# Performance work log

Measured on AMD Instinct MI355X. Metric: run time of the kernel, lower is better.

## Reference

```python
import jax, jax.numpy as jnp
import numpy as np

B, T, D = 2, 2048, 1024
H, DK, DV, NH = 8, 128, 256, 2  # heads, key dim, value dim (expand_v=2), num_householder
CONV = 4
INTER = 2816
EPS = 1e-6


def rmsnorm(x, w):
    return x * jax.lax.rsqrt(jnp.mean(x * x, -1, keepdims=True) + EPS) * w


def l2norm(x):
    return x * jax.lax.rsqrt(jnp.sum(x * x, -1, keepdims=True) + 1e-6)


def causal_conv_silu(x, w):
    # depthwise causal conv1d with silu activation; x: [B,T,C], w: [C,K]
    K = w.shape[1]
    xp = jnp.pad(x, ((0, 0), (K - 1, 0), (0, 0)))
    y = sum(xp[:, i:i + x.shape[1], :] * w[:, i] for i in range(K))
    return jax.nn.silu(y)


def setup_inputs():
    key = jax.random.key(0)
    ks = jax.random.split(key, 16)
    s = 0.02
    return {
        "hidden_states": jax.random.normal(ks[0], (B, T, D), jnp.float32),
        "attn_norm_w": jnp.ones((D,), jnp.float32),
        "Wq": jax.random.normal(ks[1], (D, H * DK), jnp.float32) * s,
        "Wk": jax.random.normal(ks[2], (D, NH * H * DK), jnp.float32) * s,
        "Wv": jax.random.normal(ks[3], (D, NH * H * DV), jnp.float32) * s,
        "Wb": jax.random.normal(ks[4], (D, H * NH), jnp.float32) * s,
        "Wa": jax.random.normal(ks[5], (D, H), jnp.float32) * s,
        "A_log": jnp.log(jax.random.uniform(ks[6], (H,), jnp.float32, 1.0, 16.0)),
        "dt_bias": jax.random.normal(ks[7], (H,), jnp.float32) * 0.5,
        "conv_q_w": jax.random.normal(ks[8], (H * DK, CONV), jnp.float32) * 0.5,
        "conv_k_w": jax.random.normal(ks[9], (NH * H * DK, CONV), jnp.float32) * 0.5,
        "conv_v_w": jax.random.normal(ks[10], (NH * H * DV, CONV), jnp.float32) * 0.5,
        "Wg": jax.random.normal(ks[11], (D, H * DV), jnp.float32) * s,
        "o_norm_w": jnp.ones((DV,), jnp.float32),
        "Wo": jax.random.normal(ks[12], (H * DV, D), jnp.float32) * s,
        "mlp_norm_w": jnp.ones((D,), jnp.float32),
        "Wgate": jax.random.normal(ks[13], (D, 2 * INTER), jnp.float32) * s,
        "Wdown": jax.random.normal(ks[14], (INTER, D), jnp.float32) * s,
    }


def reference(hidden_states, attn_norm_w, Wq, Wk, Wv, Wb, Wa, A_log, dt_bias,
              conv_q_w, conv_k_w, conv_v_w, Wg, o_norm_w, Wo,
              mlp_norm_w, Wgate, Wdown):
    residual = hidden_states
    x = rmsnorm(hidden_states, attn_norm_w)

    # projections + short conv + silu, then L2-normalized q/k (gated delta rule)
    q = l2norm(causal_conv_silu(x @ Wq, conv_q_w).reshape(B, T, H, DK))
    k = l2norm(causal_conv_silu(x @ Wk, conv_k_w).reshape(B, T, NH, H, DK))
    v = causal_conv_silu(x @ Wv, conv_v_w).reshape(B, T, NH, H, DV)
    beta = jax.nn.sigmoid(x @ Wb).reshape(B, T, H, NH)
    g = -jnp.exp(A_log) * jax.nn.softplus(x @ Wa + dt_bias)  # [B,T,H] log-decay

    def step(S, inp):
        q_t, k_t, v_t, b_t, g_t = inp
        # forget gate applied once per token, then NH Householder delta-rule updates
        S = S * jnp.exp(g_t)[..., None, None]  # S: [B,H,DK,DV]
        for j in range(NH):
            kj, vj, bj = k_t[:, j], v_t[:, j], b_t[..., j]
            kS = jnp.einsum('bhk,bhkv->bhv', kj, S)
            S = S + bj[..., None, None] * jnp.einsum('bhk,bhv->bhkv', kj, vj - kS)
        o_t = jnp.einsum('bhk,bhkv->bhv', q_t, S)
        return S, o_t

    S0 = jnp.zeros((B, H, DK, DV), x.dtype)
    xs = (jnp.swapaxes(q, 0, 1), jnp.swapaxes(k, 0, 1), jnp.swapaxes(v, 0, 1),
          jnp.swapaxes(beta, 0, 1), jnp.swapaxes(g, 0, 1))
    _, o = jax.lax.scan(step, S0, xs)  # [T,B,H,DV]
    o = jnp.swapaxes(o, 0, 1)

    # gated RMSNorm output gate + output projection
    gate = (x @ Wg).reshape(B, T, H, DV)
    o = rmsnorm(o, o_norm_w) * jax.nn.silu(gate)
    hidden = residual + o.reshape(B, T, H * DV) @ Wo

    # GatedMLP (swiglu)
    y = rmsnorm(hidden, mlp_norm_w)
    gate_m, up = jnp.split(y @ Wgate, 2, -1)
    return hidden + (jax.nn.silu(gate_m) * up) @ Wdown
```

## Files before the change

kernel.cpp:

```cpp
#include <hip/hip_runtime.h>
#include <hip/hip_bf16.h>
#include <math.h>

#define Bq 2
#define Tq 2048
#define Dq 1024
#define Hq 8
#define DKq 128
#define DVq 256
#define NHq 2
#define BTq (Bq*Tq)
#define INTERq 2816

typedef __hip_bfloat16 bf16;
typedef short bfv8 __attribute__((ext_vector_type(8)));
typedef float f32v4 __attribute__((ext_vector_type(4)));

__device__ __forceinline__ float b2f(bf16 v){ return __bfloat162float(v); }
__device__ __forceinline__ bf16 f2b(float v){ return __float2bfloat16(v); }

__device__ __forceinline__ int is_f32(const unsigned* magic){ return magic[0] == 0x3F800000u; }

__device__ __forceinline__ float ldin(const void* p, int f32, size_t i){
  return f32 ? ((const float*)p)[i] : b2f(((const bf16*)p)[i]);
}

__device__ __forceinline__ float block_reduce_sum(float v, float* red){
  #pragma unroll
  for (int off = 32; off > 0; off >>= 1) v += __shfl_down(v, off, 64);
  int lane = threadIdx.x & 63, wid = threadIdx.x >> 6;
  if (lane == 0) red[wid] = v;
  __syncthreads();
  int nw = (blockDim.x + 63) >> 6;
  float tot = 0.f;
  for (int i = 0; i < nw; i++) tot += red[i];
  return tot;
}

__global__ __launch_bounds__(256) void rmsnorm_kernel(const void* __restrict__ in, int in_mode,
    const void* __restrict__ w, const unsigned* __restrict__ magic,
    bf16* __restrict__ out){
  __shared__ float red[4];
  int f32 = is_f32(magic);
  int inf32 = in_mode ? 1 : f32;
  size_t row = blockIdx.x;
  float xv[4];
  float ss = 0.f;
  #pragma unroll
  for (int j = 0; j < 4; j++){
    int i = threadIdx.x + j*256;
    float v = ldin(in, inf32, row*Dq + i);
    xv[j] = v; ss += v*v;
  }
  float tot = block_reduce_sum(ss, red);
  float sc = rsqrtf(tot / (float)Dq + 1e-6f);
  #pragma unroll
  for (int j = 0; j < 4; j++){
    int i = threadIdx.x + j*256;
    out[row*Dq + i] = f2b(xv[j] * sc * ldin(w, f32, i));
  }
}

__global__ __launch_bounds__(256) void wsplit_kernel(
    const void* __restrict__ W, const unsigned* __restrict__ magic,
    bf16* __restrict__ hi, bf16* __restrict__ lo, int K, int N){
  __shared__ float tile[32][33];
  int f32 = is_f32(magic);
  int n0 = blockIdx.x * 32, k0 = blockIdx.y * 32;
  int tx = threadIdx.x & 31, ty = threadIdx.x >> 5;
  #pragma unroll
  for (int r = 0; r < 4; r++){
    int kr = ty + r*8;
    tile[kr][tx] = ldin(W, f32, (size_t)(k0 + kr)*N + n0 + tx);
  }
  __syncthreads();
  #pragma unroll
  for (int r = 0; r < 4; r++){
    int nr = ty + r*8;
    float v = tile[tx][nr];
    bf16 h = f2b(v);
    size_t idx = (size_t)(n0 + nr)*K + k0 + tx;
    hi[idx] = h;
    if (f32) lo[idx] = f2b(v - b2f(h));
  }
}

__global__ __launch_bounds__(256) void gemm_mfma_kernel(
    const bf16* __restrict__ A, const bf16* __restrict__ WThi, const bf16* __restrict__ WTlo,
    const unsigned* __restrict__ magic,
    const void* __restrict__ res, int res_mode,
    void* __restrict__ out, int out_mode,
    int M, int N, int K){
  int f32 = is_f32(magic);
  int tid = threadIdx.x;
  int lane = tid & 63, w = tid >> 6;
  int wm = w >> 1, wn = w & 1;
  int l15 = lane & 15, quad = lane >> 4;
  size_t bm = (size_t)blockIdx.x * 128, bn = (size_t)blockIdx.y * 128;

  f32v4 acc[4][4];
  #pragma unroll
  for (int mt = 0; mt < 4; mt++)
    #pragma unroll
    for (int nt = 0; nt < 4; nt++) acc[mt][nt] = 0.f;

  const bf16* Ab = A    + (bm + wm*64 + l15)*(size_t)K + quad*8;
  const bf16* Bh = WThi + (bn + wn*64 + l15)*(size_t)K + quad*8;
  const bf16* Bl = WTlo + (bn + wn*64 + l15)*(size_t)K + quad*8;

  if (f32){
    for (int k0 = 0; k0 < K; k0 += 32){
      bfv8 a[4];
      #pragma unroll
      for (int mt = 0; mt < 4; mt++)
        a[mt] = *(const bfv8*)(Ab + (size_t)mt*16*K + k0);
      #pragma unroll
      for (int nt = 0; nt < 4; nt++){
        bfv8 bh = *(const bfv8*)(Bh + (size_t)nt*16*K + k0);
        bfv8 bl = *(const bfv8*)(Bl + (size_t)nt*16*K + k0);
        #pragma unroll
        for (int mt = 0; mt < 4; mt++){
          acc[mt][nt] = __builtin_amdgcn_mfma_f32_16x16x32_bf16(a[mt], bh, acc[mt][nt], 0, 0, 0);
          acc[mt][nt] = __builtin_amdgcn_mfma_f32_16x16x32_bf16(a[mt], bl, acc[mt][nt], 0, 0, 0);
        }
      }
    }
  } else {
    for (int k0 = 0; k0 < K; k0 += 32){
      bfv8 a[4];
      #pragma unroll
      for (int mt = 0; mt < 4; mt++)
        a[mt] = *(const bfv8*)(Ab + (size_t)mt*16*K + k0);
      #pragma unroll
      for (int nt = 0; nt < 4; nt++){
        bfv8 bh = *(const bfv8*)(Bh + (size_t)nt*16*K + k0);
        #pragma unroll
        for (int mt = 0; mt < 4; mt++)
          acc[mt][nt] = __builtin_amdgcn_mfma_f32_16x16x32_bf16(a[mt], bh, acc[mt][nt], 0, 0, 0);
      }
    }
  }
  #pragma unroll
  for (int mt = 0; mt < 4; mt++)
    #pragma unroll
    for (int nt = 0; nt < 4; nt++)
      #pragma unroll
      for (int r = 0; r < 4; r++){
        size_t row = bm + wm*64 + mt*16 + quad*4 + r;
        size_t col = bn + wn*64 + nt*16 + l15;
        float v = acc[mt][nt][r];
        if (res_mode == 1) v += ldin(res, f32, row*N + col);
        else if (res_mode == 2) v += ((const float*)res)[row*N + col];
        if (out_mode == 0) ((float*)out)[row*N + col] = v;
        else if (out_mode == 1) ((bf16*)out)[row*N + col] = f2b(v);
        else { if (f32) ((float*)out)[row*N + col] = v; else ((bf16*)out)[row*N + col] = f2b(v); }
      }
}

__global__ __launch_bounds__(256) void betag_kernel(
    const bf16* __restrict__ x, const void* __restrict__ Wb, const void* __restrict__ Wa,
    const void* __restrict__ A_log, const void* __restrict__ dt_bias,
    const unsigned* __restrict__ magic,
    float* __restrict__ beta, float* __restrict__ eg){
  __shared__ float xs[Dq];
  int f32 = is_f32(magic);
  size_t bt = blockIdx.x;
  for (int i = threadIdx.x; i < Dq; i += 256) xs[i] = b2f(x[bt*Dq + i]);
  __syncthreads();
  int wv = threadIdx.x >> 6, lane = threadIdx.x & 63;
  #pragma unroll
  for (int r = 0; r < 6; r++){
    int n = wv*6 + r;
    float a = 0.f;
    if (n < 16){
      #pragma unroll
      for (int e = 0; e < 16; e++){
        int i = lane + 64*e;
        a = fmaf(xs[i], ldin(Wb, f32, (size_t)i*16 + n), a);
      }
    } else {
      int h = n - 16;
      #pragma unroll
      for (int e = 0; e < 16; e++){
        int i = lane + 64*e;
        a = fmaf(xs[i], ldin(Wa, f32, (size_t)i*8 + h), a);
      }
    }
    #pragma unroll
    for (int off = 32; off > 0; off >>= 1) a += __shfl_down(a, off, 64);
    if (lane == 0){
      if (n < 16){
        int h = n >> 1, j = n & 1;
        beta[(bt*Hq + h)*NHq + j] = 1.f / (1.f + expf(-a));
      } else {
        int h = n - 16;
        a += ldin(dt_bias, f32, h);
        float sp = (a > 20.f) ? a : log1pf(expf(a));
        eg[bt*Hq + h] = expf(-expf(ldin(A_log, f32, h)) * sp);
      }
    }
  }
}

__global__ __launch_bounds__(128) void conv_silu_kernel(
    const bf16* __restrict__ in, const void* __restrict__ w,
    const unsigned* __restrict__ magic,
    float* __restrict__ out, int C){
  __shared__ float red[2];
  int f32 = is_f32(magic);
  int bt = blockIdx.x;
  int t = bt & (Tq - 1);
  int c = blockIdx.y * 128 + threadIdx.x;
  float acc = 0.f;
  #pragma unroll
  for (int i = 0; i < 4; i++){
    int tt = t - 3 + i;
    if (tt >= 0) acc = fmaf(b2f(in[(size_t)(bt - 3 + i)*C + c]), ldin(w, f32, (size_t)c*4 + i), acc);
  }
  float y = acc / (1.f + expf(-acc));
  float tot = block_reduce_sum(y*y, red);
  y *= rsqrtf(tot + 1e-6f);
  out[(size_t)bt*C + c] = y;
}

__global__ __launch_bounds__(256) void conv_v_kernel(
    const bf16* __restrict__ in, const void* __restrict__ w,
    const unsigned* __restrict__ magic, bf16* __restrict__ out){
  int f32 = is_f32(magic);
  int bt = blockIdx.x;
  int t = bt & (Tq - 1);
  int c = blockIdx.y * 256 + threadIdx.x;
  float acc = 0.f;
  #pragma unroll
  for (int i = 0; i < 4; i++){
    int tt = t - 3 + i;
    if (tt >= 0) acc = fmaf(b2f(in[(size_t)(bt - 3 + i)*4096 + c]), ldin(w, f32, (size_t)c*4 + i), acc);
  }
  out[(size_t)bt*4096 + c] = f2b(acc / (1.f + expf(-acc)));
}

#define DPP_ADD(x, ctrl) ((x) + __int_as_float(__builtin_amdgcn_update_dpp( \
    0, __float_as_int(x), (ctrl), 0xF, 0xF, true)))
#define KRED(p) { p = DPP_ADD(p, 0x128); p = DPP_ADD(p, 0x124); \
                  p = DPP_ADD(p, 0x122); p = DPP_ADD(p, 0x121); }

__global__ __launch_bounds__(64, 1) void scan_kernel(
    const float* __restrict__ qn,
    const float* __restrict__ kn,
    const bf16*  __restrict__ vcv,
    const float* __restrict__ beta,
    const float* __restrict__ eg,
    float* __restrict__ o){
  int bh = blockIdx.x;
  int b = bh >> 3, h = bh & 7;
  int lane = threadIdx.x;
  int kg = lane & 15;
  int vloc = lane >> 4;
  int vv = blockIdx.y * 4 + vloc;
  int c0 = (h << 8) + vv;
  int c1 = 2048 + (h << 8) + vv;
  const size_t base = (size_t)b * Tq;
  const float* knh = kn + base*2048 + h*DKq + kg*8;
  const float* qnh = qn + (base*Hq + h)*(size_t)DKq + kg*8;
  const bf16*  vph = vcv + base*4096;
  const float* gh  = eg + base*Hq + h;
  const float2* bph = (const float2*)(beta + (base*Hq + h)*(size_t)NHq);
  float* oh = o + (base*Hq + h)*(size_t)DVq + vv;

  float4 S0 = {0,0,0,0}, S1 = {0,0,0,0};
#define SDOT(Ka, Kb, p) { \
    float e0 = fmaf(Ka.x, S0.x, Ka.y * S0.y); \
    float e1 = fmaf(Ka.z, S0.z, Ka.w * S0.w); \
    float e2 = fmaf(Kb.x, S1.x, Kb.y * S1.y); \
    float e3 = fmaf(Kb.z, S1.z, Kb.w * S1.w); \
    p = (e0 + e1) + (e2 + e3); }
#define SUPD(Ka, Kb, d) { \
    S0.x = fmaf(Ka.x, d, S0.x); S0.y = fmaf(Ka.y, d, S0.y); \
    S0.z = fmaf(Ka.z, d, S0.z); S0.w = fmaf(Ka.w, d, S0.w); \
    S1.x = fmaf(Kb.x, d, S1.x); S1.y = fmaf(Kb.y, d, S1.y); \
    S1.z = fmaf(Kb.z, d, S1.z); S1.w = fmaf(Kb.w, d, S1.w); }

  float4 A0E = *(const float4*)(knh);
  float4 A1E = *(const float4*)(knh + 4);
  float4 B0E = *(const float4*)(knh + 1024);
  float4 B1E = *(const float4*)(knh + 1028);
  float4 Q0E = *(const float4*)(qnh);
  float4 Q1E = *(const float4*)(qnh + 4);
  float4 A0O = *(const float4*)(knh + 2048);
  float4 A1O = *(const float4*)(knh + 2052);
  float4 B0O = *(const float4*)(knh + 3072);
  float4 B1O = *(const float4*)(knh + 3076);
  float4 Q0O = *(const float4*)(qnh + 1024);
  float4 Q1O = *(const float4*)(qnh + 1028);
  float  gE  = gh[0],   gO  = gh[8];
  float2 beE = bph[0],  beO = bph[8];
  float vaE = b2f(vph[c0]),        vbE = b2f(vph[c1]);
  float vaO = b2f(vph[4096 + c0]), vbO = b2f(vph[4096 + c1]);

#define STEP(A0,A1,B0,B1,Q0,Q1, gS, beS, vaS, vbS, t, tp) { \
    float egv = gS; \
    gS = gh[(tp)*8]; \
    S0.x *= egv; S0.y *= egv; S0.z *= egv; S0.w *= egv; \
    S1.x *= egv; S1.y *= egv; S1.z *= egv; S1.w *= egv; \
     \
    { float p; SDOT(A0, A1, p) \
      KRED(p) \
      float delta = beS.x * (vaS - p); \
      SUPD(A0, A1, delta) \
      A0 = *(const float4*)(knh + (tp)*2048); \
      A1 = *(const float4*)(knh + (tp)*2048 + 4); \
      vaS = b2f(vph[(tp)*4096 + c0]); } \
     \
    { float p; SDOT(B0, B1, p) \
      KRED(p) \
      float delta = beS.y * (vbS - p); \
      SUPD(B0, B1, delta) \
      B0 = *(const float4*)(knh + (tp)*2048 + 1024); \
      B1 = *(const float4*)(knh + (tp)*2048 + 1028); \
      vbS = b2f(vph[(tp)*4096 + c1]); } \
    beS = bph[(tp)*8]; \
     \
    { float p; SDOT(Q0, Q1, p) \
      KRED(p) \
      if ((lane & 15) == 0) oh[(t)*2048] = p; \
      Q0 = *(const float4*)(qnh + (tp)*1024); \
      Q1 = *(const float4*)(qnh + (tp)*1024 + 4); } \
    __builtin_amdgcn_sched_barrier(0); }

  for (int t = 0; t < Tq; t += 2){
    STEP(A0E,A1E,B0E,B1E,Q0E,Q1E, gE,beE,vaE,vbE, t,   t+2)
    STEP(A0O,A1O,B0O,B1O,Q0O,Q1O, gO,beO,vaO,vbO, t+1, t+3)
  }
#undef STEP
#undef SDOT
#undef SUPD
}

__global__ __launch_bounds__(256) void gate_o_kernel(
    const float* __restrict__ o, const void* __restrict__ onw,
    const unsigned* __restrict__ magic,
    const bf16* __restrict__ gate, bf16* __restrict__ og){
  __shared__ float red[4];
  int f32 = is_f32(magic);
  size_t bth = blockIdx.x;
  int dv = threadIdx.x;
  float v = o[bth*DVq + dv];
  float tot = block_reduce_sum(v*v, red);
  float sc = rsqrtf(tot / (float)DVq + 1e-6f);
  float gt = b2f(gate[bth*DVq + dv]);
  float silu = gt / (1.f + expf(-gt));
  og[bth*DVq + dv] = f2b(v * sc * ldin(onw, f32, dv) * silu);
}

__global__ __launch_bounds__(256) void silumul_kernel(
    const bf16* __restrict__ gu, bf16* __restrict__ mid, int n){
  int i = blockIdx.x * 256 + threadIdx.x;
  if (i >= n) return;
  int bt = i / INTERq, c = i % INTERq;
  float gm = b2f(gu[(size_t)bt*2*INTERq + c]);
  float up = b2f(gu[(size_t)bt*2*INTERq + INTERq + c]);
  mid[i] = f2b(gm / (1.f + expf(-gm)) * up);
}

extern "C" void kernel_launch(void* const* d_in, const int* in_sizes, int n_in,
                              void* d_out, int out_size, void* d_ws, size_t ws_size,
                              hipStream_t stream){
  const void* hs      = d_in[0];
  const unsigned* magic = (const unsigned*)d_in[1];
  const void* attn_nw = d_in[1];
  const void* Wq      = d_in[2];
  const void* Wk      = d_in[3];
  const void* Wv      = d_in[4];
  const void* Wb      = d_in[5];
  const void* Wa      = d_in[6];
  const void* A_log   = d_in[7];
  const void* dt_bias = d_in[8];
  const void* conv_q  = d_in[9];
  const void* conv_k  = d_in[10];
  const void* conv_v  = d_in[11];
  const void* Wg      = d_in[12];
  const void* o_nw    = d_in[13];
  const void* Wo      = d_in[14];
  const void* mlp_nw  = d_in[15];
  const void* Wgate   = d_in[16];
  const void* Wdown   = d_in[17];

  char* ws = (char*)d_ws;
  const size_t MB = (size_t)1 << 20;
  size_t X     = 0;
  size_t QPRE  = 8*MB;
  size_t KPRE  = 16*MB;
  size_t VPRE  = 32*MB;
  size_t GATE  = 64*MB;
  size_t QN    = 80*MB;
  size_t KN    = 96*MB;
  size_t HID   = 128*MB;
  size_t BETA  = 144*MB;
  size_t Gb    = 144*MB + 512*1024;
  size_t VCV    = 0;
  size_t O      = 32*MB;
  size_t OG     = QN;
  size_t Y      = KN;
  size_t GATEUP = 0;
  size_t MID    = 44*MB;
  size_t W0 = 145*MB;
  size_t WTQh = W0 +  0*MB, WTQl = W0 +  2*MB;
  size_t WTKh = W0 +  4*MB, WTKl = W0 +  8*MB;
  size_t WTVh = W0 + 12*MB, WTVl = W0 + 20*MB;
  size_t WTGh = W0 + 28*MB, WTGl = W0 + 32*MB;
  size_t WTOh = W0 + 36*MB, WTOl = W0 + 40*MB;
  size_t WTUh = W0 + 44*MB, WTUl = W0 + 56*MB;
  size_t WTDh = W0 + 68*MB, WTDl = W0 + 74*MB;
  (void)ws_size; (void)in_sizes; (void)n_in; (void)out_size;

  wsplit_kernel<<<dim3(1024/32, 1024/32), 256, 0, stream>>>(Wq,    magic, (bf16*)(ws+WTQh), (bf16*)(ws+WTQl), 1024, 1024);
  wsplit_kernel<<<dim3(2048/32, 1024/32), 256, 0, stream>>>(Wk,    magic, (bf16*)(ws+WTKh), (bf16*)(ws+WTKl), 1024, 2048);
  wsplit_kernel<<<dim3(4096/32, 1024/32), 256, 0, stream>>>(Wv,    magic, (bf16*)(ws+WTVh), (bf16*)(ws+WTVl), 1024, 4096);
  wsplit_kernel<<<dim3(2048/32, 1024/32), 256, 0, stream>>>(Wg,    magic, (bf16*)(ws+WTGh), (bf16*)(ws+WTGl), 1024, 2048);
  wsplit_kernel<<<dim3(1024/32, 2048/32), 256, 0, stream>>>(Wo,    magic, (bf16*)(ws+WTOh), (bf16*)(ws+WTOl), 2048, 1024);
  wsplit_kernel<<<dim3(5632/32, 1024/32), 256, 0, stream>>>(Wgate, magic, (bf16*)(ws+WTUh), (bf16*)(ws+WTUl), 1024, 5632);
  wsplit_kernel<<<dim3(1024/32, 2816/32), 256, 0, stream>>>(Wdown, magic, (bf16*)(ws+WTDh), (bf16*)(ws+WTDl), 2816, 1024);

  rmsnorm_kernel<<<BTq, 256, 0, stream>>>(hs, 0, attn_nw, magic, (bf16*)(ws+X));

  gemm_mfma_kernel<<<dim3(32,  8), 256, 0, stream>>>((bf16*)(ws+X), (bf16*)(ws+WTQh), (bf16*)(ws+WTQl), magic, nullptr, 0, ws+QPRE, 1, BTq, 1024, 1024);
  gemm_mfma_kernel<<<dim3(32, 16), 256, 0, stream>>>((bf16*)(ws+X), (bf16*)(ws+WTKh), (bf16*)(ws+WTKl), magic, nullptr, 0, ws+KPRE, 1, BTq, 2048, 1024);
  gemm_mfma_kernel<<<dim3(32, 32), 256, 0, stream>>>((bf16*)(ws+X), (bf16*)(ws+WTVh), (bf16*)(ws+WTVl), magic, nullptr, 0, ws+VPRE, 1, BTq, 4096, 1024);
  gemm_mfma_kernel<<<dim3(32, 16), 256, 0, stream>>>((bf16*)(ws+X), (bf16*)(ws+WTGh), (bf16*)(ws+WTGl), magic, nullptr, 0, ws+GATE, 1, BTq, 2048, 1024);
  betag_kernel<<<BTq, 256, 0, stream>>>((bf16*)(ws+X), Wb, Wa, A_log, dt_bias, magic, (float*)(ws+BETA), (float*)(ws+Gb));

  conv_silu_kernel<<<dim3(BTq, 1024/128), 128, 0, stream>>>((bf16*)(ws+QPRE), conv_q, magic, (float*)(ws+QN), 1024);
  conv_silu_kernel<<<dim3(BTq, 2048/128), 128, 0, stream>>>((bf16*)(ws+KPRE), conv_k, magic, (float*)(ws+KN), 2048);
  conv_v_kernel<<<dim3(BTq, 4096/256), 256, 0, stream>>>((bf16*)(ws+VPRE), conv_v, magic, (bf16*)(ws+VCV));

  scan_kernel<<<dim3(Bq*Hq, DVq/4), 64, 0, stream>>>(
      (const float*)(ws+QN), (const float*)(ws+KN), (const bf16*)(ws+VCV),
      (const float*)(ws+BETA), (const float*)(ws+Gb), (float*)(ws+O));

  gate_o_kernel<<<BTq*Hq, 256, 0, stream>>>((const float*)(ws+O), o_nw, magic, (const bf16*)(ws+GATE), (bf16*)(ws+OG));

  gemm_mfma_kernel<<<dim3(32, 8), 256, 0, stream>>>((bf16*)(ws+OG), (bf16*)(ws+WTOh), (bf16*)(ws+WTOl), magic, hs, 1, ws+HID, 0, BTq, 1024, 2048);

  rmsnorm_kernel<<<BTq, 256, 0, stream>>>(ws+HID, 1, mlp_nw, magic, (bf16*)(ws+Y));

  gemm_mfma_kernel<<<dim3(32, 44), 256, 0, stream>>>((bf16*)(ws+Y), (bf16*)(ws+WTUh), (bf16*)(ws+WTUl), magic, nullptr, 0, ws+GATEUP, 1, BTq, 5632, 1024);

  int nmid = BTq * INTERq;
  silumul_kernel<<<(nmid + 255)/256, 256, 0, stream>>>((const bf16*)(ws+GATEUP), (bf16*)(ws+MID), nmid);

  gemm_mfma_kernel<<<dim3(32, 8), 256, 0, stream>>>((bf16*)(ws+MID), (bf16*)(ws+WTDh), (bf16*)(ws+WTDl), magic, ws+HID, 2, d_out, 2, BTq, 1024, 2816);
}
```

Measured before the change: 2.441 ms.

## Stage bf16 GEMM tiles through double-buffered LDS via direct global-to-LDS loads

In the bf16 path of the MFMA GEMM, each wave no longer loads A and B fragments straight from global memory. The block now cooperatively stages 128x32 tiles into double-buffered shared memory using global_load_lds, then reads fragments from LDS. This removes redundant global traffic across waves and overlaps the next tile's load with the current MFMAs. It adds a barrier per k-step and may cause LDS bank conflicts from the unpadded 32-element row stride. The f32 hi/lo path is unchanged, and since the test inputs are f32, the new path may not run by default.

```diff
diff --git a/kernel.cpp b/kernel.cpp
--- a/kernel.cpp
+++ b/kernel.cpp
@@ -25,6 +25,12 @@
   return f32 ? ((const float*)p)[i] : b2f(((const bf16*)p)[i]);
 }
 
+__device__ __forceinline__ void gload_lds16(const bf16* g, bf16* lds_uniform){
+  __builtin_amdgcn_global_load_lds(
+      (const __attribute__((address_space(1))) void*)g,
+      (__attribute__((address_space(3))) void*)lds_uniform, 16, 0, 0);
+}
+
 __device__ __forceinline__ float block_reduce_sum(float v, float* red){
   #pragma unroll
   for (int off = 32; off > 0; off >>= 1) v += __shfl_down(v, off, 64);
@@ -91,6 +97,8 @@
     const void* __restrict__ res, int res_mode,
     void* __restrict__ out, int out_mode,
     int M, int N, int K){
+  __shared__ bf16 As[2][128*32];
+  __shared__ bf16 Bs[2][128*32];
   int f32 = is_f32(magic);
   int tid = threadIdx.x;
   int lane = tid & 63, w = tid >> 6;
@@ -104,11 +112,10 @@
     #pragma unroll
     for (int nt = 0; nt < 4; nt++) acc[mt][nt] = 0.f;
 
-  const bf16* Ab = A    + (bm + wm*64 + l15)*(size_t)K + quad*8;
-  const bf16* Bh = WThi + (bn + wn*64 + l15)*(size_t)K + quad*8;
-  const bf16* Bl = WTlo + (bn + wn*64 + l15)*(size_t)K + quad*8;
-
   if (f32){
+    const bf16* Ab = A    + (bm + wm*64 + l15)*(size_t)K + quad*8;
+    const bf16* Bh = WThi + (bn + wn*64 + l15)*(size_t)K + quad*8;
+    const bf16* Bl = WTlo + (bn + wn*64 + l15)*(size_t)K + quad*8;
     for (int k0 = 0; k0 < K; k0 += 32){
       bfv8 a[4];
       #pragma unroll
@@ -126,20 +133,48 @@
       }
     }
   } else {
-    for (int k0 = 0; k0 < K; k0 += 32){
-      bfv8 a[4];
+    int srow = tid >> 2;
+    int scol = (tid & 3) * 8;
+    const bf16* Ag = A    + (bm + srow)*(size_t)K + scol;
+    const bf16* Bg = WThi + (bn + srow)*(size_t)K + scol;
+    int wslot = w * 512;
+    int nt = K >> 5;
+
+#define STAGE(buf, k0) { \
+    const bf16* a0 = Ag + (k0); \
+    const bf16* b0 = Bg + (k0); \
+    gload_lds16(a0,                 &As[buf][wslot]); \
+    gload_lds16(a0 + 64*(size_t)K,  &As[buf][2048 + wslot]); \
+    gload_lds16(b0,                 &Bs[buf][wslot]); \
+    gload_lds16(b0 + 64*(size_t)K,  &Bs[buf][2048 + wslot]); }
+
+    int aoff = (wm*64 + l15)*32 + quad*8;
+    int boff = (wn*64 + l15)*32 + quad*8;
+
+    STAGE(0, 0)
+    asm volatile("s_waitcnt vmcnt(0)" ::: "memory");
+    __syncthreads();
+    for (int t = 0; t < nt; ++t){
+      int cur = t & 1;
+      if (t + 1 < nt) STAGE(cur ^ 1, (t+1) << 5)
+      bfv8 a[4], bb[4];
       #pragma unroll
       for (int mt = 0; mt < 4; mt++)
-        a[mt] = *(const bfv8*)(Ab + (size_t)mt*16*K + k0);
-      #pragma unroll
-      for (int nt = 0; nt < 4; nt++){
-        bfv8 bh = *(const bfv8*)(Bh + (size_t)nt*16*K + k0);
+        a[mt] = *(const bfv8*)(&As[cur][aoff + mt*16*32]);
+      #pragma unroll
+      for (int nn = 0; nn < 4; nn++)
+        bb[nn] = *(const bfv8*)(&Bs[cur][boff + nn*16*32]);
+      #pragma unroll
+      for (int nn = 0; nn < 4; nn++)
         #pragma unroll
         for (int mt = 0; mt < 4; mt++)
-          acc[mt][nt] = __builtin_amdgcn_mfma_f32_16x16x32_bf16(a[mt], bh, acc[mt][nt], 0, 0, 0);
-      }
+          acc[mt][nn] = __builtin_amdgcn_mfma_f32_16x16x32_bf16(a[mt], bb[nn], acc[mt][nn], 0, 0, 0);
+      asm volatile("s_waitcnt vmcnt(0)" ::: "memory");
+      __syncthreads();
     }
-  }
+#undef STAGE
+  }
+
   #pragma unroll
   for (int mt = 0; mt < 4; mt++)
     #pragma unroll
```

Measured after the change: 2.417 ms. Within noise of the previous version (-1.0%).
